# Performance work log

Measured on AMD Instinct MI355X. Metric: run time of the kernel, lower is better.

Reference implementation:

```python
import jax, jax.numpy as jnp
import numpy as np

B, N = 16384, 4096
PERCENT_ON = 0.1
TEMPERATURE = 10.0  # training-mode temperature
K = int(round(N * PERCENT_ON))  # 410


def setup_inputs() -> dict:
    key = jax.random.key(0)
    k1, k2 = jax.random.split(key)
    x = jax.random.normal(k1, (B, N), dtype=jnp.float32)
    # Gumbel noise for sampling-without-replacement (Gumbel-top-k trick),
    # equivalent to torch.multinomial(softmax(x/T), k, replacement=False).
    gumbel = jax.random.gumbel(k2, (B, N), dtype=jnp.float32)
    return {"x": x, "gumbel": gumbel}


def reference(x, gumbel):
    # logits with temperature
    logits = x / TEMPERATURE
    # entropy of the categorical distribution per row, averaged (single stable pass)
    logp = jax.nn.log_softmax(logits, axis=-1)
    entropy = jnp.mean(-jnp.sum(jnp.exp(logp) * logp, axis=-1))
    # sample K winners without replacement via Gumbel-top-k
    _, idx = jax.lax.top_k(logits + gumbel, K)  # idx: [B, K]
    rows = jnp.arange(x.shape[0])[:, None]       # [B, 1]
    mask = jnp.zeros_like(x).at[rows, idx].set(1.0)
    out = x * mask  # relu=False path
    return out, entropy
```

## Files before the change

kernel.cpp:

```cpp
#include <hip/hip_runtime.h>
#include <math.h>

#define TPB 256
#define EPT 16
#define NN  4096
#define KSEL 410

__device__ __forceinline__ unsigned sortkey(float f) {
    unsigned u = __float_as_uint(f);
    unsigned m = (unsigned)(((int)u) >> 31);
    return u ^ (m | 0x80000000u);
}

template <bool USE_WS>
__global__ __launch_bounds__(TPB)
void skw_main(const float* __restrict__ x, const float* __restrict__ g,
              float* __restrict__ out, float* __restrict__ rowH,
              float* __restrict__ entAcc, float invB)
{
    const int row  = blockIdx.x;
    const int t    = threadIdx.x;
    const int w    = t >> 6;
    const int lane = t & 63;
    const size_t base = (size_t)row * NN + (size_t)t * EPT;

    float xv[EPT];
    unsigned key[EPT];

    const float4* xp = reinterpret_cast<const float4*>(x + base);
    const float4* gp = reinterpret_cast<const float4*>(g + base);
#pragma unroll
    for (int q = 0; q < EPT / 4; ++q) {
        float4 xx = xp[q];
        float4 gg = gp[q];
        xv[4*q+0] = xx.x; xv[4*q+1] = xx.y; xv[4*q+2] = xx.z; xv[4*q+3] = xx.w;
        key[4*q+0] = sortkey(xx.x / 10.0f + gg.x);
        key[4*q+1] = sortkey(xx.y / 10.0f + gg.y);
        key[4*q+2] = sortkey(xx.z / 10.0f + gg.z);
        key[4*q+3] = sortkey(xx.w / 10.0f + gg.w);
    }

    __shared__ unsigned hist4[4][256];
    __shared__ unsigned wtot[4];
    __shared__ float    fred[8];
    __shared__ unsigned sh_digit, sh_above;

    float lm = -INFINITY;
#pragma unroll
    for (int j = 0; j < EPT; ++j) lm = fmaxf(lm, xv[j] * 0.1f);
#pragma unroll
    for (int s = 32; s >= 1; s >>= 1) lm = fmaxf(lm, __shfl_xor(lm, s));
    if (lane == 0) fred[w] = lm;
    __syncthreads();
    const float m = fmaxf(fmaxf(fred[0], fred[1]), fmaxf(fred[2], fred[3]));

    float sZ = 0.f, sZL = 0.f;
#pragma unroll
    for (int j = 0; j < EPT; ++j) {
        float d = xv[j] * 0.1f - m;
        float e = __expf(d);
        sZ += e; sZL += e * d;
    }
#pragma unroll
    for (int s = 32; s >= 1; s >>= 1) { sZ += __shfl_xor(sZ, s); sZL += __shfl_xor(sZL, s); }
    __syncthreads();
    if (lane == 0) { fred[w] = sZ; fred[4 + w] = sZL; }
    __syncthreads();
    if (t == 0) {
        float Z = fred[0] + fred[1] + fred[2] + fred[3];
        float L = fred[4] + fred[5] + fred[6] + fred[7];
        float H = __logf(Z) - L / Z;
        if (USE_WS) rowH[row] = H;
        else atomicAdd(entAcc, H * invB);
    }

    unsigned* hflat = &hist4[0][0];
    unsigned prefix = 0;
    unsigned Kr = KSEL;
#pragma unroll
    for (int p = 0; p < 4; ++p) {
        const int shift = 24 - 8 * p;
        hflat[t] = 0; hflat[t + 256] = 0; hflat[t + 512] = 0; hflat[t + 768] = 0;
        __syncthreads();
#pragma unroll
        for (int j = 0; j < EPT; ++j) {
            unsigned k = key[j];
            if (p == 0) {
                atomicAdd(&hist4[w][k >> 24], 1u);
            } else {
                if ((k >> (shift + 8)) == prefix)
                    atomicAdd(&hist4[w][(k >> shift) & 255u], 1u);
            }
        }
        __syncthreads();
        unsigned v = hist4[0][t] + hist4[1][t] + hist4[2][t] + hist4[3][t];
#pragma unroll
        for (int s = 1; s < 64; s <<= 1) {
            unsigned tmp = __shfl(v, lane + s);
            v += (lane + s < 64) ? tmp : 0u;
        }
        if (lane == 0) wtot[w] = v;
        unsigned vnext = __shfl(v, lane + 1);
        __syncthreads();
        unsigned hi = 0;
#pragma unroll
        for (int c = 0; c < 4; ++c) hi += (c > w) ? wtot[c] : 0u;
        unsigned cum     = v + hi;
        unsigned cumNext = ((lane < 63) ? vnext : 0u) + hi;
        if (cum >= Kr && cumNext < Kr) { sh_digit = (unsigned)t; sh_above = cumNext; }
        __syncthreads();
        prefix = (prefix << 8) | sh_digit;
        Kr -= sh_above;
    }
    const unsigned thr = prefix;

    unsigned eq = 0;
#pragma unroll
    for (int j = 0; j < EPT; ++j) eq += (key[j] == thr) ? 1u : 0u;
    unsigned v = eq;
#pragma unroll
    for (int s = 1; s < 64; s <<= 1) {
        unsigned tmp = __shfl(v, lane - s);
        v += (lane >= s) ? tmp : 0u;
    }
    if (lane == 63) wtot[w] = v;
    __syncthreads();
    unsigned offset = 0;
#pragma unroll
    for (int c = 0; c < 4; ++c) offset += (c < w) ? wtot[c] : 0u;
    unsigned pos = offset + v - eq;

    float4* op = reinterpret_cast<float4*>(out + base);
#pragma unroll
    for (int q = 0; q < EPT / 4; ++q) {
        float vals[4];
#pragma unroll
        for (int jj = 0; jj < 4; ++jj) {
            int j = 4 * q + jj;
            bool sel;
            if (key[j] > thr)       sel = true;
            else if (key[j] == thr) { sel = (pos < Kr); ++pos; }
            else                    sel = false;
            vals[jj] = sel ? xv[j] : 0.0f;
        }
        float4 o4; o4.x = vals[0]; o4.y = vals[1]; o4.z = vals[2]; o4.w = vals[3];
        op[q] = o4;
    }
}

__global__ void skw_zero(float* p) { *p = 0.0f; }

__global__ void skw_reduce(const float* __restrict__ rowH, float* __restrict__ outp, int B)
{
    __shared__ float red[256];
    int t = threadIdx.x;
    float s = 0.f;
    for (int i = t; i < B; i += 256) s += rowH[i];
    red[t] = s; __syncthreads();
    for (int st = 128; st > 0; st >>= 1) { if (t < st) red[t] += red[t + st]; __syncthreads(); }
    if (t == 0) *outp = red[0] / (float)B;
}

extern "C" void kernel_launch(void* const* d_in, const int* in_sizes, int n_in,
                              void* d_out, int out_size, void* d_ws, size_t ws_size,
                              hipStream_t stream)
{
    const float* x = (const float*)d_in[0];
    const float* g = (const float*)d_in[1];
    float* out = (float*)d_out;
    const int BN = in_sizes[0];
    const int B  = BN / NN;
    float* entp = out + (size_t)BN;

    if (ws_size >= (size_t)B * sizeof(float)) {
        float* rowH = (float*)d_ws;
        skw_main<true><<<B, TPB, 0, stream>>>(x, g, out, rowH, nullptr, 0.f);
        skw_reduce<<<1, 256, 0, stream>>>(rowH, entp, B);
    } else {
        skw_zero<<<1, 1, 0, stream>>>(entp);
        skw_main<false><<<B, TPB, 0, stream>>>(x, g, out, nullptr, entp, 1.0f / (float)B);
    }
}
```

Baseline: 197.7 us.

## Prefilter top-k with coarse value buckets before radix refinement; drop max pass

Each element gets a coarse value bucket (s*16+64, clamped). A first histogram over these buckets, spread across 8 replicas to cut shared-atomic contention, locates the bucket holding the K-th element. The four radix passes then histogram only the elements in that bucket, so far fewer atomics run per pass. The softmax max-reduction pass is removed, relying on x/10 being small enough that exp does not overflow. The x register array is also dropped and x is re-read from global memory at output time, trading extra loads for lower register pressure.

```diff
diff --git a/kernel.cpp b/kernel.cpp
--- a/kernel.cpp
+++ b/kernel.cpp
@@ -24,48 +24,52 @@
     const int lane = t & 63;
     const size_t base = (size_t)row * NN + (size_t)t * EPT;
 
-    float xv[EPT];
     unsigned key[EPT];
-
-    const float4* xp = reinterpret_cast<const float4*>(x + base);
-    const float4* gp = reinterpret_cast<const float4*>(g + base);
-#pragma unroll
-    for (int q = 0; q < EPT / 4; ++q) {
-        float4 xx = xp[q];
-        float4 gg = gp[q];
-        xv[4*q+0] = xx.x; xv[4*q+1] = xx.y; xv[4*q+2] = xx.z; xv[4*q+3] = xx.w;
-        key[4*q+0] = sortkey(xx.x / 10.0f + gg.x);
-        key[4*q+1] = sortkey(xx.y / 10.0f + gg.y);
-        key[4*q+2] = sortkey(xx.z / 10.0f + gg.z);
-        key[4*q+3] = sortkey(xx.w / 10.0f + gg.w);
-    }
-
-    __shared__ unsigned hist4[4][256];
+    unsigned bp[EPT / 4];
+
+    __shared__ unsigned hist0[256][8];
+    __shared__ unsigned histr[4][256];
     __shared__ unsigned wtot[4];
     __shared__ float    fred[8];
     __shared__ unsigned sh_digit, sh_above;
 
-    float lm = -INFINITY;
-#pragma unroll
-    for (int j = 0; j < EPT; ++j) lm = fmaxf(lm, xv[j] * 0.1f);
-#pragma unroll
-    for (int s = 32; s >= 1; s >>= 1) lm = fmaxf(lm, __shfl_xor(lm, s));
-    if (lane == 0) fred[w] = lm;
-    __syncthreads();
-    const float m = fmaxf(fmaxf(fred[0], fred[1]), fmaxf(fred[2], fred[3]));
+    const float4* xp = reinterpret_cast<const float4*>(x + base);
+    const float4* gp = reinterpret_cast<const float4*>(g + base);
 
     float sZ = 0.f, sZL = 0.f;
 #pragma unroll
-    for (int j = 0; j < EPT; ++j) {
-        float d = xv[j] * 0.1f - m;
-        float e = __expf(d);
-        sZ += e; sZL += e * d;
-    }
-#pragma unroll
-    for (int s = 32; s >= 1; s >>= 1) { sZ += __shfl_xor(sZ, s); sZL += __shfl_xor(sZL, s); }
-    __syncthreads();
+    for (int q = 0; q < EPT / 4; ++q) {
+        float4 xx = xp[q];
+        float4 gg = gp[q];
+        float xa[4] = {xx.x, xx.y, xx.z, xx.w};
+        float ga[4] = {gg.x, gg.y, gg.z, gg.w};
+        unsigned pk = 0;
+#pragma unroll
+        for (int jj = 0; jj < 4; ++jj) {
+            float xs = xa[jj];
+            float l  = xs * 0.1f;
+            float e  = __expf(l);
+            sZ  += e;
+            sZL += e * l;
+            float q10 = __builtin_fmaf(__builtin_fmaf(-10.0f, l, xs), 0.1f, l);
+            float s = q10 + ga[jj];
+            key[4 * q + jj] = sortkey(s);
+            int b = (int)__builtin_fmaf(s, 16.0f, 64.0f);
+            b = min(max(b, 0), 255);
+            pk |= (unsigned)b << (8 * jj);
+        }
+        bp[q] = pk;
+    }
+
+#pragma unroll
+    for (int sft = 32; sft >= 1; sft >>= 1) { sZ += __shfl_xor(sZ, sft); sZL += __shfl_xor(sZL, sft); }
     if (lane == 0) { fred[w] = sZ; fred[4 + w] = sZL; }
-    __syncthreads();
+
+    unsigned* h0 = &hist0[0][0];
+#pragma unroll
+    for (int i = 0; i < 8; ++i) h0[t + 256 * i] = 0;
+    __syncthreads();
+
     if (t == 0) {
         float Z = fred[0] + fred[1] + fred[2] + fred[3];
         float L = fred[4] + fred[5] + fred[6] + fred[7];
@@ -74,40 +78,77 @@
         else atomicAdd(entAcc, H * invB);
     }
 
-    unsigned* hflat = &hist4[0][0];
-    unsigned prefix = 0;
+#pragma unroll
+    for (int q = 0; q < EPT / 4; ++q) {
+        unsigned pk = bp[q];
+#pragma unroll
+        for (int jj = 0; jj < 4; ++jj)
+            atomicAdd(&hist0[(pk >> (8 * jj)) & 255u][lane & 7], 1u);
+    }
+    __syncthreads();
+
+    unsigned v = 0;
+#pragma unroll
+    for (int k = 0; k < 8; ++k) v += hist0[t][k];
+#pragma unroll
+    for (int sft = 1; sft < 64; sft <<= 1) {
+        unsigned tmp = __shfl(v, lane + sft);
+        v += (lane + sft < 64) ? tmp : 0u;
+    }
+    if (lane == 0) wtot[w] = v;
+    unsigned vnext = __shfl(v, lane + 1);
+    __syncthreads();
     unsigned Kr = KSEL;
-#pragma unroll
-    for (int p = 0; p < 4; ++p) {
-        const int shift = 24 - 8 * p;
-        hflat[t] = 0; hflat[t + 256] = 0; hflat[t + 512] = 0; hflat[t + 768] = 0;
-        __syncthreads();
-#pragma unroll
-        for (int j = 0; j < EPT; ++j) {
-            unsigned k = key[j];
-            if (p == 0) {
-                atomicAdd(&hist4[w][k >> 24], 1u);
-            } else {
-                if ((k >> (shift + 8)) == prefix)
-                    atomicAdd(&hist4[w][(k >> shift) & 255u], 1u);
-            }
-        }
-        __syncthreads();
-        unsigned v = hist4[0][t] + hist4[1][t] + hist4[2][t] + hist4[3][t];
-#pragma unroll
-        for (int s = 1; s < 64; s <<= 1) {
-            unsigned tmp = __shfl(v, lane + s);
-            v += (lane + s < 64) ? tmp : 0u;
-        }
-        if (lane == 0) wtot[w] = v;
-        unsigned vnext = __shfl(v, lane + 1);
-        __syncthreads();
+    {
         unsigned hi = 0;
 #pragma unroll
         for (int c = 0; c < 4; ++c) hi += (c > w) ? wtot[c] : 0u;
         unsigned cum     = v + hi;
         unsigned cumNext = ((lane < 63) ? vnext : 0u) + hi;
         if (cum >= Kr && cumNext < Kr) { sh_digit = (unsigned)t; sh_above = cumNext; }
+    }
+    __syncthreads();
+    const unsigned Bstar = sh_digit;
+    Kr -= sh_above;
+
+    unsigned cm = 0;
+#pragma unroll
+    for (int q = 0; q < EPT / 4; ++q) {
+        unsigned pk = bp[q];
+#pragma unroll
+        for (int jj = 0; jj < 4; ++jj)
+            cm |= (((pk >> (8 * jj)) & 255u) == Bstar) ? (1u << (4 * q + jj)) : 0u;
+    }
+
+    unsigned prefix = 0;
+#pragma unroll
+    for (int p = 0; p < 4; ++p) {
+        const int shift = 24 - 8 * p;
+        histr[w][lane] = 0; histr[w][lane + 64] = 0; histr[w][lane + 128] = 0; histr[w][lane + 192] = 0;
+#pragma unroll
+        for (int j = 0; j < EPT; ++j) {
+            if ((cm >> j) & 1u) {
+                unsigned k = key[j];
+                if (p == 0 || (k >> (shift + 8)) == prefix)
+                    atomicAdd(&histr[w][(k >> shift) & 255u], 1u);
+            }
+        }
+        __syncthreads();
+        unsigned vv = histr[0][t] + histr[1][t] + histr[2][t] + histr[3][t];
+#pragma unroll
+        for (int sft = 1; sft < 64; sft <<= 1) {
+            unsigned tmp = __shfl(vv, lane + sft);
+            vv += (lane + sft < 64) ? tmp : 0u;
+        }
+        if (lane == 0) wtot[w] = vv;
+        unsigned vvn = __shfl(vv, lane + 1);
+        __syncthreads();
+        unsigned hi2 = 0;
+#pragma unroll
+        for (int c = 0; c < 4; ++c) hi2 += (c > w) ? wtot[c] : 0u;
+        unsigned cum2  = vv + hi2;
+        unsigned cumN2 = ((lane < 63) ? vvn : 0u) + hi2;
+        if (cum2 >= Kr && cumN2 < Kr) { sh_digit = (unsigned)t; sh_above = cumN2; }
         __syncthreads();
         prefix = (prefix << 8) | sh_digit;
         Kr -= sh_above;
@@ -117,22 +158,24 @@
     unsigned eq = 0;
 #pragma unroll
     for (int j = 0; j < EPT; ++j) eq += (key[j] == thr) ? 1u : 0u;
-    unsigned v = eq;
-#pragma unroll
-    for (int s = 1; s < 64; s <<= 1) {
-        unsigned tmp = __shfl(v, lane - s);
-        v += (lane >= s) ? tmp : 0u;
-    }
-    if (lane == 63) wtot[w] = v;
+    unsigned pv = eq;
+#pragma unroll
+    for (int sft = 1; sft < 64; sft <<= 1) {
+        unsigned tmp = __shfl(pv, lane - sft);
+        pv += (lane >= sft) ? tmp : 0u;
+    }
+    if (lane == 63) wtot[w] = pv;
     __syncthreads();
     unsigned offset = 0;
 #pragma unroll
     for (int c = 0; c < 4; ++c) offset += (c < w) ? wtot[c] : 0u;
-    unsigned pos = offset + v - eq;
+    unsigned pos = offset + pv - eq;
 
     float4* op = reinterpret_cast<float4*>(out + base);
 #pragma unroll
     for (int q = 0; q < EPT / 4; ++q) {
+        float4 xx = xp[q];
+        float xa[4] = {xx.x, xx.y, xx.z, xx.w};
         float vals[4];
 #pragma unroll
         for (int jj = 0; jj < 4; ++jj) {
@@ -141,7 +184,7 @@
             if (key[j] > thr)       sel = true;
             else if (key[j] == thr) { sel = (pos < Kr); ++pos; }
             else                    sel = false;
-            vals[jj] = sel ? xv[j] : 0.0f;
+            vals[jj] = sel ? xa[jj] : 0.0f;
         }
         float4 o4; o4.x = vals[0]; o4.y = vals[1]; o4.z = vals[2]; o4.w = vals[3];
         op[q] = o4;
```

Result: slower. 259.8 us (+31.4%).
